# Performance work log

Hardware: AMD Instinct MI355X
Metric: run time of the kernel (lower is better)

The kernel has to match this reference:

```python
import jax, jax.numpy as jnp
import numpy as np

B, S, H = 2, 2048, 1024
NH, DH = 16, 64  # num heads, head dim

def setup_inputs() -> dict:
    key = jax.random.key(0)
    ks = jax.random.split(key, 4)
    scale = 0.02
    return {
        "hidden_states": jax.random.normal(ks[0], (B, S, H), dtype=jnp.float32),
        "attention_mask": jnp.zeros((B, 1, 1, S), dtype=jnp.float32),  # additive mask
        "Wq": jax.random.normal(ks[1], (H, H), dtype=jnp.float32) * scale,
        "bq": jnp.zeros((H,), dtype=jnp.float32),
        "Wk": jax.random.normal(ks[2], (H, H), dtype=jnp.float32) * scale,
        "bk": jnp.zeros((H,), dtype=jnp.float32),
        "Wv": jax.random.normal(ks[3], (H, H), dtype=jnp.float32) * scale,
        "bv": jnp.zeros((H,), dtype=jnp.float32),
    }

def _split_heads(x):
    # [B,S,H] -> [B,NH,S,DH]
    return x.reshape(B, S, NH, DH).transpose(0, 2, 1, 3)

def reference(hidden_states, attention_mask, Wq, bq, Wk, bk, Wv, bv):
    q = _split_heads(hidden_states @ Wq + bq)
    k = _split_heads(hidden_states @ Wk + bk)
    v = _split_heads(hidden_states @ Wv + bv)
    # scores: [B,NH,S,S]
    scores = jnp.einsum('bhqd,bhkd->bhqk', q, k) / jnp.asarray(np.sqrt(DH), scores_dtype := q.dtype)
    scores = scores + attention_mask  # additive mask broadcast
    probs = jax.nn.softmax(scores, axis=-1)
    out = jnp.einsum('bhqk,bhkd->bhqd', probs, v)  # [B,NH,S,DH]
    out = out.transpose(0, 2, 1, 3).reshape(B, S, H)
    return out
```

## Files before the change

kernel.cpp:

```cpp
#include <hip/hip_runtime.h>
#include <hip/hip_bf16.h>

#define Bn  2
#define Sn  2048
#define Hn  1024
#define NHn 16
#define DHn 64
#define Mn  (Bn * Sn)

typedef __attribute__((ext_vector_type(4)))  float    f32x4;
typedef __attribute__((ext_vector_type(16))) float    f32x16;
typedef __attribute__((ext_vector_type(8)))  _Float16 h8;
typedef __attribute__((ext_vector_type(4)))  _Float16 h4;
typedef __attribute__((ext_vector_type(2)))  __fp16   fp16x2;
typedef __attribute__((ext_vector_type(2)))  unsigned int u32x2;

union H2PK { fp16x2 v; unsigned int u; };
union U4H8 { unsigned int u[4]; h8 v; };

#define MFMA16F(a, b, c) __builtin_amdgcn_mfma_f32_16x16x32_f16(a, b, c, 0, 0, 0)
#define MFMA32F(a, b, c) __builtin_amdgcn_mfma_f32_32x32x16_f16(a, b, c, 0, 0, 0)

__device__ __forceinline__ void glds16(const void* g, void* l) {
    __builtin_amdgcn_global_load_lds(
        (const __attribute__((address_space(1))) unsigned int*)g,
        (__attribute__((address_space(3))) unsigned int*)l, 16, 0, 0);
}

__global__ __launch_bounds__(256) void prep(
    const float* __restrict__ X, const float* __restrict__ W0,
    const float* __restrict__ W1, const float* __restrict__ W2,
    _Float16* __restrict__ Xh, _Float16* __restrict__ WT)
{
    const int bid = blockIdx.x;
    const int tid = threadIdx.x;
    __shared__ float Ws[64][65];

    if (bid < 4096) {
        const int i = bid * 256 + tid;
        float4 x = ((const float4*)X)[i];
        h4 o;
        o[0] = (_Float16)x.x; o[1] = (_Float16)x.y;
        o[2] = (_Float16)x.z; o[3] = (_Float16)x.w;
        *(h4*)&Xh[(size_t)i * 4] = o;
        return;
    }

    const int wb = bid - 4096;
    const int which = wb >> 8;
    const int rem = wb & 255;
    const int k0 = ((rem >> 4) & 15) * 64;
    const int n0 = (rem & 15) * 64;
    const float* W = (which == 0) ? W0 : (which == 1 ? W1 : W2);
    _Float16* O = WT + (size_t)which * Hn * Hn;

#pragma unroll
    for (int it = 0; it < 4; ++it) {
        const int idx = tid + 256 * it;
        const int row = idx >> 4, c4 = (idx & 15) * 4;
        float4 w = *(const float4*)&W[(size_t)(k0 + row) * Hn + n0 + c4];
        Ws[row][c4 + 0] = w.x; Ws[row][c4 + 1] = w.y;
        Ws[row][c4 + 2] = w.z; Ws[row][c4 + 3] = w.w;
    }
    __syncthreads();
#pragma unroll
    for (int it = 0; it < 16; ++it) {
        const int e = tid + 256 * it;
        const int k = e & 63, n = e >> 6;
        O[(size_t)(n0 + n) * Hn + k0 + k] = (_Float16)Ws[k][n];
    }
}

__global__ __launch_bounds__(256) void qkv_mfma(
    const _Float16* __restrict__ Xh, const _Float16* __restrict__ WTA,
    const float* __restrict__ b0, const float* __restrict__ b1,
    const float* __restrict__ b2,
    _Float16* __restrict__ Qh, _Float16* __restrict__ Kh,
    _Float16* __restrict__ VTh)
{
    const int which = blockIdx.z;
    const _Float16* WT = WTA + (size_t)which * Hn * Hn;
    const float* bias = (which == 0) ? b0 : (which == 1 ? b1 : b2);
    _Float16* Dst = (which == 0) ? Qh : (which == 1 ? Kh : VTh);

    const int m0 = blockIdx.x * 128;
    const int n0 = blockIdx.y * 128;
    const int tid  = threadIdx.x;
    const int wid  = tid >> 6;
    const int lane = tid & 63;
    const int l16  = lane & 15;
    const int quad = lane >> 4;
    const int wm = wid >> 1, wn = wid & 1;

    __shared__ _Float16 Ah[128 * 32], Bh[128 * 32];

    f32x4 acc[4][4];
#pragma unroll
    for (int i = 0; i < 4; ++i)
#pragma unroll
        for (int j = 0; j < 4; ++j) acc[i][j] = (f32x4){0.f, 0.f, 0.f, 0.f};

    for (int kt = 0; kt < Hn / 32; ++kt) {
        const int k0 = kt * 32;
        __syncthreads();
#pragma unroll
        for (int c = 0; c < 2; ++c) {
            const int idx = (wid * 2 + c) * 64 + lane;
            const int row = idx >> 2;
            const int cg  = (idx & 3) ^ (row & 3);
            glds16(&Xh[(size_t)(m0 + row) * Hn + k0 + cg * 8],
                   &Ah[(wid * 2 + c) * 512]);
            glds16(&WT[(size_t)(n0 + row) * Hn + k0 + cg * 8],
                   &Bh[(wid * 2 + c) * 512]);
        }
        __syncthreads();

        h8 xa[4], wb[4];
#pragma unroll
        for (int t = 0; t < 4; ++t) {
            const int ar = wm * 64 + t * 16 + l16;
            const int br = wn * 64 + t * 16 + l16;
            xa[t] = *(const h8*)&Ah[ar * 32 + ((quad ^ (ar & 3)) * 8)];
            wb[t] = *(const h8*)&Bh[br * 32 + ((quad ^ (br & 3)) * 8)];
        }
        if (which < 2) {
#pragma unroll
            for (int i = 0; i < 4; ++i)
#pragma unroll
                for (int j = 0; j < 4; ++j)
                    acc[i][j] = MFMA16F(xa[i], wb[j], acc[i][j]);
        } else {
#pragma unroll
            for (int i = 0; i < 4; ++i)
#pragma unroll
                for (int j = 0; j < 4; ++j)
                    acc[i][j] = MFMA16F(wb[i], xa[j], acc[i][j]);
        }
    }

    if (which < 2) {
#pragma unroll
        for (int j = 0; j < 4; ++j) {
            const int n = n0 + wn * 64 + j * 16 + l16;
            const float bv = bias[n];
            const int hh = n >> 6, dd = n & 63;
#pragma unroll
            for (int i = 0; i < 4; ++i) {
                const int mb = m0 + wm * 64 + i * 16 + quad * 4;
#pragma unroll
                for (int r = 0; r < 4; ++r) {
                    const int m = mb + r;
                    const int b = m >> 11, s = m & (Sn - 1);
                    Dst[(((size_t)b * NHn + hh) * Sn + s) * DHn + dd] =
                        (_Float16)(acc[i][j][r] + bv);
                }
            }
        }
    } else {
#pragma unroll
        for (int i = 0; i < 4; ++i) {
#pragma unroll
            for (int r = 0; r < 4; ++r) {
                const int n = n0 + wn * 64 + i * 16 + quad * 4 + r;
                const float bv = bias[n];
                const int hh = n >> 6, dd = n & 63;
#pragma unroll
                for (int j = 0; j < 4; ++j) {
                    const int m = m0 + wm * 64 + j * 16 + l16;
                    const int b = m >> 11, s = m & (Sn - 1);
                    Dst[(((size_t)b * NHn + hh) * DHn + dd) * Sn + s] =
                        (_Float16)(acc[i][j][r] + bv);
                }
            }
        }
    }
}

__global__ __launch_bounds__(256, 2) void attn(
    const _Float16* __restrict__ Qh, const _Float16* __restrict__ Kh,
    const _Float16* __restrict__ VTh, const float* __restrict__ mask,
    float* __restrict__ Out)
{
    const int flat = blockIdx.x + 16 * blockIdx.y + 256 * blockIdx.z;
    const int bh   = ((flat & 7) << 2) | ((flat >> 3) & 3);
    const int qb   = flat >> 5;
    const int b = bh >> 4, h = bh & 15;

    const int tid  = threadIdx.x;
    const int wid  = tid >> 6;
    const int lane = tid & 63;
    const int l32  = lane & 31;
    const int hi   = lane >> 5;

    __shared__ __align__(16) _Float16 Kb[4][4096];
    __shared__ __align__(16) _Float16 Vb[4][4096];
    __shared__ float4 Ml4[Sn / 4];
    const float* Ml = (const float*)Ml4;

    const int q0 = qb * 128 + wid * 32;

    const float4* mg = (const float4*)(mask + (size_t)b * Sn);
    float4 m0v = mg[tid], m1v = mg[tid + 256];

    const size_t qbase = ((size_t)bh * Sn + q0 + l32) * DHn;
    h8 qf[4];
#pragma unroll
    for (int kd = 0; kd < 4; ++kd)
        qf[kd] = *(const h8*)&Qh[qbase + kd * 16 + hi * 8];

    asm volatile("s_waitcnt vmcnt(0)" ::: "memory");

    {
        const float L2E = 1.44269504088896340736f;
        float4 a0 = {m0v.x * L2E, m0v.y * L2E, m0v.z * L2E, m0v.w * L2E};
        float4 a1 = {m1v.x * L2E, m1v.y * L2E, m1v.z * L2E, m1v.w * L2E};
        Ml4[tid] = a0;
        Ml4[tid + 256] = a1;
    }

    const _Float16* Kg = Kh  + (size_t)bh * Sn * DHn;
    const _Float16* Vg = VTh + (size_t)bh * DHn * Sn;

    auto stage = [&](int kt, int buf) {
        const int koff = kt * 64;
#pragma unroll
        for (int c = 0; c < 2; ++c) {
            const int idx = (wid * 2 + c) * 64 + lane;
            const int row = idx >> 3;
            const int cg  = (idx & 7) ^ (row & 7);
            glds16(&Kg[(size_t)(koff + row) * DHn + cg * 8],
                   &Kb[buf][(wid * 2 + c) * 512]);
            glds16(&Vg[(size_t)row * Sn + koff + cg * 8],
                   &Vb[buf][(wid * 2 + c) * 512]);
        }
    };

    stage(0, 0);
    stage(1, 1);

    f32x16 sA[2], sB[2], o[2], acc_l;
#pragma unroll
    for (int dt = 0; dt < 2; ++dt) o[dt] = (f32x16)(0.f);
    acc_l = (f32x16)(0.f);

    h8 ones;
#pragma unroll
    for (int j = 0; j < 8; ++j) ones[j] = (_Float16)1.0f;

    auto qkt = [&](f32x16 (&s)[2], int buf) {
        __builtin_amdgcn_s_setprio(1);
#pragma unroll
        for (int t = 0; t < 2; ++t) {
            f32x16 c = (f32x16)(0.f);
#pragma unroll
            for (int kd = 0; kd < 4; ++kd) {
                const int row = t * 32 + l32;
                h8 kf = *(const h8*)&Kb[buf][row * 64 +
                                             (((kd * 2 + hi) ^ (row & 7)) * 8)];
                c = MFMA32F(kf, qf[kd], c);
            }
            s[t] = c;
        }
        __builtin_amdgcn_s_setprio(0);
    };

    auto sm_pv = [&](f32x16 (&s)[2], int kt, int buf) {
        const float SC = 0.18033688011112042f;
        unsigned int pk[2][4][2];
#pragma unroll
        for (int t = 0; t < 2; ++t) {
#pragma unroll
            for (int g = 0; g < 4; ++g) {
                float4 mv = *(const float4*)&Ml[kt * 64 + t * 32 + hi * 4 + g * 8];
                const float p0 = __builtin_amdgcn_exp2f(s[t][g * 4 + 0] * SC + mv.x);
                const float p1 = __builtin_amdgcn_exp2f(s[t][g * 4 + 1] * SC + mv.y);
                const float p2 = __builtin_amdgcn_exp2f(s[t][g * 4 + 2] * SC + mv.z);
                const float p3 = __builtin_amdgcn_exp2f(s[t][g * 4 + 3] * SC + mv.w);
                H2PK u0, u1;
                u0.v = __builtin_amdgcn_cvt_pkrtz(p0, p1);
                u1.v = __builtin_amdgcn_cvt_pkrtz(p2, p3);
                pk[t][g][0] = u0.u;
                pk[t][g][1] = u1.u;
            }
        }

        __builtin_amdgcn_s_setprio(1);
#pragma unroll
        for (int ks = 0; ks < 4; ++ks) {
            const int t = ks >> 1, ge = (ks & 1) * 2;
            u32x2 rA = __builtin_amdgcn_permlane32_swap(
                pk[t][ge][0], pk[t][ge + 1][0], false, false);
            u32x2 rB = __builtin_amdgcn_permlane32_swap(
                pk[t][ge][1], pk[t][ge + 1][1], false, false);
            U4H8 w;
            w.u[0] = rA[0]; w.u[1] = rB[0]; w.u[2] = rA[1]; w.u[3] = rB[1];
            acc_l = MFMA32F(w.v, ones, acc_l);
#pragma unroll
            for (int dt = 0; dt < 2; ++dt) {
                const int row = dt * 32 + l32;
                h8 vf = *(const h8*)&Vb[buf][row * 64 +
                                             (((ks * 2 + hi) ^ (row & 7)) * 8)];
                o[dt] = MFMA32F(w.v, vf, o[dt]);
            }
        }
        __builtin_amdgcn_s_setprio(0);
    };

    asm volatile("s_waitcnt vmcnt(4) lgkmcnt(0)" ::: "memory");
    __builtin_amdgcn_s_barrier();
    qkt(sA, 0);

    auto iter = [&](int kt, f32x16 (&scur)[2], f32x16 (&snxt)[2]) {
        stage(kt + 2, (kt + 2) & 3);
        asm volatile("s_waitcnt vmcnt(4)" ::: "memory");
        __builtin_amdgcn_s_barrier();
        qkt(snxt, (kt + 1) & 3);
        sm_pv(scur, kt, kt & 3);
    };

    for (int kt = 0; kt < 30; kt += 2) {
        iter(kt,     sA, sB);
        iter(kt + 1, sB, sA);
    }
    asm volatile("s_waitcnt vmcnt(0)" ::: "memory");
    __builtin_amdgcn_s_barrier();
    qkt(sB, 31 & 3);
    sm_pv(sA, 30, 30 & 3);
    sm_pv(sB, 31, 31 & 3);

#pragma unroll
    for (int g2 = 0; g2 < 4; ++g2) {
#pragma unroll
        for (int e = 0; e < 4; ++e) {
            const int r = g2 * 4 + e;
            const int q = q0 + 4 * hi + 8 * g2 + e;
            const size_t ob = ((size_t)b * Sn + q) * Hn + h * DHn;
            const float sc = 1.0f / acc_l[r];
#pragma unroll
            for (int dt = 0; dt < 2; ++dt)
                Out[ob + dt * 32 + l32] = o[dt][r] * sc;
        }
    }
}

extern "C" void kernel_launch(void* const* d_in, const int* in_sizes, int n_in,
                              void* d_out, int out_size, void* d_ws, size_t ws_size,
                              hipStream_t stream) {
    const float* X    = (const float*)d_in[0];
    const float* mask = (const float*)d_in[1];
    const float* Wq   = (const float*)d_in[2];
    const float* bq   = (const float*)d_in[3];
    const float* Wk   = (const float*)d_in[4];
    const float* bk   = (const float*)d_in[5];
    const float* Wv   = (const float*)d_in[6];
    const float* bv   = (const float*)d_in[7];
    float* out = (float*)d_out;

    const size_t NE = (size_t)Mn * Hn;
    _Float16* Xh  = (_Float16*)d_ws;
    _Float16* WT  = Xh + NE;
    _Float16* Qh  = WT + (size_t)3 * Hn * Hn;
    _Float16* Kh  = Qh + NE;
    _Float16* VTh = Kh + NE;

    prep<<<dim3(4096 + 768), dim3(256), 0, stream>>>(X, Wq, Wk, Wv, Xh, WT);

    dim3 g1(Mn / 128, Hn / 128, 3), b1(256);
    qkv_mfma<<<g1, b1, 0, stream>>>(Xh, WT, bq, bk, bv, Qh, Kh, VTh);

    dim3 g2(Sn / 128, NHn, Bn), b2(256);
    attn<<<g2, b2, 0, stream>>>(Qh, Kh, VTh, mask, out);
}
```

Before: 177.2 us.

## Double-buffer projection GEMM and fold softmax scale and mask into QK accumulator

The QKV projection GEMM now double-buffers its LDS tiles, so global loads for the next k-tile overlap the MFMAs on the current tile. The softmax scale (1/sqrt(d) times log2 e) is folded into Q at projection time. The log2-scaled mask is used as the initial QK^T accumulator, which removes a multiply-add per score in the softmax loop. In exchange, the GEMM uses twice the LDS and adds an extra barrier per iteration, and Q is stored pre-scaled in fp16, which slightly changes rounding.

```diff
diff --git a/kernel.cpp b/kernel.cpp
--- a/kernel.cpp
+++ b/kernel.cpp
@@ -20,6 +20,9 @@
 
 #define MFMA16F(a, b, c) __builtin_amdgcn_mfma_f32_16x16x32_f16(a, b, c, 0, 0, 0)
 #define MFMA32F(a, b, c) __builtin_amdgcn_mfma_f32_32x32x16_f16(a, b, c, 0, 0, 0)
+
+#define SCFULL 0.18033688011112042f
+#define L2E    1.44269504088896340736f
 
 __device__ __forceinline__ void glds16(const void* g, void* l) {
     __builtin_amdgcn_global_load_lds(
@@ -92,7 +95,7 @@
     const int quad = lane >> 4;
     const int wm = wid >> 1, wn = wid & 1;
 
-    __shared__ _Float16 Ah[128 * 32], Bh[128 * 32];
+    __shared__ _Float16 Ah[2][128 * 32], Bh[2][128 * 32];
 
     f32x4 acc[4][4];
 #pragma unroll
@@ -100,28 +103,40 @@
 #pragma unroll
         for (int j = 0; j < 4; ++j) acc[i][j] = (f32x4){0.f, 0.f, 0.f, 0.f};
 
-    for (int kt = 0; kt < Hn / 32; ++kt) {
+    auto stage = [&](int kt, int bb) {
         const int k0 = kt * 32;
-        __syncthreads();
 #pragma unroll
         for (int c = 0; c < 2; ++c) {
             const int idx = (wid * 2 + c) * 64 + lane;
             const int row = idx >> 2;
             const int cg  = (idx & 3) ^ (row & 3);
             glds16(&Xh[(size_t)(m0 + row) * Hn + k0 + cg * 8],
-                   &Ah[(wid * 2 + c) * 512]);
+                   &Ah[bb][(wid * 2 + c) * 512]);
             glds16(&WT[(size_t)(n0 + row) * Hn + k0 + cg * 8],
-                   &Bh[(wid * 2 + c) * 512]);
-        }
-        __syncthreads();
-
+                   &Bh[bb][(wid * 2 + c) * 512]);
+        }
+    };
+
+    stage(0, 0);
+
+    for (int kt = 0; kt < Hn / 32; ++kt) {
+        if (kt + 1 < Hn / 32) {
+            stage(kt + 1, (kt + 1) & 1);
+            asm volatile("s_waitcnt vmcnt(4)" ::: "memory");
+        } else {
+            asm volatile("s_waitcnt vmcnt(0)" ::: "memory");
+        }
+        __builtin_amdgcn_s_barrier();
+        asm volatile("" ::: "memory");
+
+        const int bb = kt & 1;
         h8 xa[4], wb[4];
 #pragma unroll
         for (int t = 0; t < 4; ++t) {
             const int ar = wm * 64 + t * 16 + l16;
             const int br = wn * 64 + t * 16 + l16;
-            xa[t] = *(const h8*)&Ah[ar * 32 + ((quad ^ (ar & 3)) * 8)];
-            wb[t] = *(const h8*)&Bh[br * 32 + ((quad ^ (br & 3)) * 8)];
+            xa[t] = *(const h8*)&Ah[bb][ar * 32 + ((quad ^ (ar & 3)) * 8)];
+            wb[t] = *(const h8*)&Bh[bb][br * 32 + ((quad ^ (br & 3)) * 8)];
         }
         if (which < 2) {
 #pragma unroll
@@ -136,8 +151,11 @@
                 for (int j = 0; j < 4; ++j)
                     acc[i][j] = MFMA16F(wb[i], xa[j], acc[i][j]);
         }
-    }
-
+        __builtin_amdgcn_s_barrier();
+        asm volatile("" ::: "memory");
+    }
+
+    const float oscale = (which == 0) ? SCFULL : 1.0f;
     if (which < 2) {
 #pragma unroll
         for (int j = 0; j < 4; ++j) {
@@ -152,7 +170,7 @@
                     const int m = mb + r;
                     const int b = m >> 11, s = m & (Sn - 1);
                     Dst[(((size_t)b * NHn + hh) * Sn + s) * DHn + dd] =
-                        (_Float16)(acc[i][j][r] + bv);
+                        (_Float16)((acc[i][j][r] + bv) * oscale);
                 }
             }
         }
@@ -211,7 +229,6 @@
     asm volatile("s_waitcnt vmcnt(0)" ::: "memory");
 
     {
-        const float L2E = 1.44269504088896340736f;
         float4 a0 = {m0v.x * L2E, m0v.y * L2E, m0v.z * L2E, m0v.w * L2E};
         float4 a1 = {m1v.x * L2E, m1v.y * L2E, m1v.z * L2E, m1v.w * L2E};
         Ml4[tid] = a0;
@@ -247,11 +264,17 @@
 #pragma unroll
     for (int j = 0; j < 8; ++j) ones[j] = (_Float16)1.0f;
 
-    auto qkt = [&](f32x16 (&s)[2], int buf) {
+    auto qkt = [&](f32x16 (&s)[2], int buf, int ktile) {
         __builtin_amdgcn_s_setprio(1);
 #pragma unroll
         for (int t = 0; t < 2; ++t) {
-            f32x16 c = (f32x16)(0.f);
+            f32x16 c;
+#pragma unroll
+            for (int g = 0; g < 4; ++g) {
+                float4 mv = *(const float4*)&Ml[ktile * 64 + t * 32 + hi * 4 + g * 8];
+                c[g * 4 + 0] = mv.x; c[g * 4 + 1] = mv.y;
+                c[g * 4 + 2] = mv.z; c[g * 4 + 3] = mv.w;
+            }
 #pragma unroll
             for (int kd = 0; kd < 4; ++kd) {
                 const int row = t * 32 + l32;
@@ -264,18 +287,16 @@
         __builtin_amdgcn_s_setprio(0);
     };
 
-    auto sm_pv = [&](f32x16 (&s)[2], int kt, int buf) {
-        const float SC = 0.18033688011112042f;
+    auto sm_pv = [&](f32x16 (&s)[2], int buf) {
         unsigned int pk[2][4][2];
 #pragma unroll
         for (int t = 0; t < 2; ++t) {
 #pragma unroll
             for (int g = 0; g < 4; ++g) {
-                float4 mv = *(const float4*)&Ml[kt * 64 + t * 32 + hi * 4 + g * 8];
-                const float p0 = __builtin_amdgcn_exp2f(s[t][g * 4 + 0] * SC + mv.x);
-                const float p1 = __builtin_amdgcn_exp2f(s[t][g * 4 + 1] * SC + mv.y);
-                const float p2 = __builtin_amdgcn_exp2f(s[t][g * 4 + 2] * SC + mv.z);
-                const float p3 = __builtin_amdgcn_exp2f(s[t][g * 4 + 3] * SC + mv.w);
+                const float p0 = __builtin_amdgcn_exp2f(s[t][g * 4 + 0]);
+                const float p1 = __builtin_amdgcn_exp2f(s[t][g * 4 + 1]);
+                const float p2 = __builtin_amdgcn_exp2f(s[t][g * 4 + 2]);
+                const float p3 = __builtin_amdgcn_exp2f(s[t][g * 4 + 3]);
                 H2PK u0, u1;
                 u0.v = __builtin_amdgcn_cvt_pkrtz(p0, p1);
                 u1.v = __builtin_amdgcn_cvt_pkrtz(p2, p3);
@@ -308,14 +329,14 @@
 
     asm volatile("s_waitcnt vmcnt(4) lgkmcnt(0)" ::: "memory");
     __builtin_amdgcn_s_barrier();
-    qkt(sA, 0);
+    qkt(sA, 0, 0);
 
     auto iter = [&](int kt, f32x16 (&scur)[2], f32x16 (&snxt)[2]) {
         stage(kt + 2, (kt + 2) & 3);
         asm volatile("s_waitcnt vmcnt(4)" ::: "memory");
         __builtin_amdgcn_s_barrier();
-        qkt(snxt, (kt + 1) & 3);
-        sm_pv(scur, kt, kt & 3);
+        qkt(snxt, (kt + 1) & 3, kt + 1);
+        sm_pv(scur, kt & 3);
     };
 
     for (int kt = 0; kt < 30; kt += 2) {
@@ -324,9 +345,9 @@
     }
     asm volatile("s_waitcnt vmcnt(0)" ::: "memory");
     __builtin_amdgcn_s_barrier();
-    qkt(sB, 31 & 3);
-    sm_pv(sA, 30, 30 & 3);
-    sm_pv(sB, 31, 31 & 3);
+    qkt(sB, 31 & 3, 31);
+    sm_pv(sA, 30 & 3);
+    sm_pv(sB, 31 & 3);
 
 #pragma unroll
     for (int g2 = 0; g2 < 4; ++g2) {
```

Result: slower. 185.5 us (+4.7%).
